# Kernel tuning notes

Hardware: AMD Instinct MI355X
Metric: run time of the kernel (lower is better)

## Reference

```python
import jax, jax.numpy as jnp
import numpy as np

N = 50000
E = 800000
FIN = 128
H = 2
C = 64
OUT = 40
NEG_SLOPE = 0.2
BN_EPS = 1e-5


def setup_inputs() -> dict:
    key = jax.random.key(0)
    ks = jax.random.split(key, 16)
    inv = lambda f: 1.0 / np.sqrt(f)
    return {
        "x": jax.random.normal(ks[0], (N, FIN), jnp.float32),
        "edge_index": jax.random.randint(ks[1], (2, E), 0, N, dtype=jnp.int64),
        "W1": jax.random.normal(ks[2], (FIN, H * C), jnp.float32) * inv(FIN),
        "att_src1": jax.random.normal(ks[3], (H, C), jnp.float32) * inv(C),
        "att_dst1": jax.random.normal(ks[4], (H, C), jnp.float32) * inv(C),
        "b1": jax.random.normal(ks[5], (H * C,), jnp.float32) * 0.1,
        "bn_gamma": jnp.ones((H * C,), jnp.float32),
        "bn_beta": jnp.zeros((H * C,), jnp.float32),
        "bn_mean": jax.random.normal(ks[6], (H * C,), jnp.float32) * 0.1,
        "bn_var": jax.random.uniform(ks[7], (H * C,), jnp.float32) + 0.5,
        "W2": jax.random.normal(ks[8], (H * C, H * C), jnp.float32) * inv(H * C),
        "att_src2": jax.random.normal(ks[9], (H, C), jnp.float32) * inv(C),
        "att_dst2": jax.random.normal(ks[10], (H, C), jnp.float32) * inv(C),
        "b2": jax.random.normal(ks[11], (H * C,), jnp.float32) * 0.1,
        "Wf": jax.random.normal(ks[12], (H * C, OUT), jnp.float32) * inv(H * C),
        "bf": jax.random.normal(ks[13], (OUT,), jnp.float32) * 0.1,
    }


def _gat_conv(x, src, dst, W, att_src, att_dst, b):
    """PyG GATConv (concat=True): per-edge attention, segment softmax over dst, scatter-sum."""
    n = x.shape[0]
    h = (x @ W).reshape(n, H, C)                       # [N,H,C]
    a_src = jnp.sum(h * att_src, axis=-1)              # [N,H]
    a_dst = jnp.sum(h * att_dst, axis=-1)              # [N,H]
    e = jax.nn.leaky_relu(a_src[src] + a_dst[dst], NEG_SLOPE)   # [E,H]
    m = jax.ops.segment_max(e, dst, num_segments=n)    # [N,H]
    m = jnp.where(jnp.isfinite(m), m, 0.0)
    ex = jnp.exp(e - m[dst])                           # [E,H]
    denom = jax.ops.segment_sum(ex, dst, num_segments=n)
    alpha = ex / (denom[dst] + 1e-16)                  # [E,H]
    out = jax.ops.segment_sum(alpha[:, :, None] * h[src], dst, num_segments=n)  # [N,H,C]
    return out.reshape(n, H * C) + b


def reference(x, edge_index, W1, att_src1, att_dst1, b1, bn_gamma, bn_beta,
              bn_mean, bn_var, W2, att_src2, att_dst2, b2, Wf, bf):
    n = x.shape[0]
    # GATConv default add_self_loops=True
    loops = jnp.arange(n, dtype=edge_index.dtype)
    src = jnp.concatenate([edge_index[0], loops])
    dst = jnp.concatenate([edge_index[1], loops])

    x1 = _gat_conv(x, src, dst, W1, att_src1, att_dst1, b1)
    # BatchNorm1d (inference: running stats)
    x1 = (x1 - bn_mean) * jax.lax.rsqrt(bn_var + BN_EPS) * bn_gamma + bn_beta
    x1 = jax.nn.elu(x1)
    # dropout is identity in eval mode
    x2 = _gat_conv(x1, src, dst, W2, att_src2, att_dst2, b2)

    xj = jnp.maximum(x1, x2)                           # JumpingKnowledge 'max'
    logits = xj @ Wf + bf
    return jax.nn.log_softmax(logits, axis=1)
```

## Files before the change

### kernel.cpp

```cpp
#include <hip/hip_runtime.h>

#define NN 50000
#define EE 800000
#define ETOT 850000
#define NEG 0.2f
#define BNEPS 1e-5f
#define OUTC 40
#define MSHIFT 20.0f
#define PSZ 6250
#define NCHUNK 416
#define CHSZ 2044
#define ELLW 64

typedef unsigned short ushort_t;
typedef unsigned char uchar_t;
typedef unsigned int uint32;
typedef long long ll_t;

typedef __attribute__((ext_vector_type(8))) short short8;
typedef __attribute__((ext_vector_type(4))) float f32x4;
typedef __attribute__((ext_vector_type(2))) float f32x2;

__device__ __forceinline__ float bf2f(ushort_t u){ return __uint_as_float(((uint32)u)<<16); }
__device__ __forceinline__ float2 upk2(uint32 v){
  return make_float2(__uint_as_float(v<<16), __uint_as_float(v & 0xffff0000u));
}
__device__ __forceinline__ ushort_t f2bf(float f){
  uint32 u = __float_as_uint(f);
  uint32 r = ((u>>16)&1u) + 0x7fffu;
  return (ushort_t)((u + r)>>16);
}
__device__ __forceinline__ float ldf(const void* p, int i, bool f32){
  return f32 ? ((const float*)p)[i] : bf2f(((const ushort_t*)p)[i]);
}

__device__ __forceinline__ uchar_t enc_fp8(float v){
#if __has_builtin(__builtin_amdgcn_cvt_pk_fp8_f32)
  int p = __builtin_amdgcn_cvt_pk_fp8_f32(v, v, 0, false);
  return (uchar_t)(p & 0xFF);
#else
  float a = fabsf(v);
  uint32 s = (v < 0.f) ? 0x80u : 0u;
  if (a < 0.0009765625f) return (uchar_t)s;
  a = fminf(a, 448.f);
  int e; float m = frexpf(a, &e);
  int E = e + 6;
  uint32 mant;
  if (E <= 0){
    mant = (uint32)lrintf(a * 512.f);
    if (mant > 7) return (uchar_t)(s | 0x08u);
    return (uchar_t)(s | mant);
  }
  mant = (uint32)lrintf(m * 16.f);
  if (mant >= 16){ mant = 8; E += 1; }
  if (E > 15){ E = 15; mant = 14; }
  return (uchar_t)(s | ((uint32)E<<3) | (mant - 8));
#endif
}
__device__ __forceinline__ float2 dec_fp8x2(ushort_t h){
#if __has_builtin(__builtin_amdgcn_cvt_pk_f32_fp8)
  f32x2 r = __builtin_amdgcn_cvt_pk_f32_fp8((uint32)h, false);
  return make_float2(r[0], r[1]);
#else
  float o[2];
  #pragma unroll
  for (int i=0;i<2;i++){
    uint32 v = (h >> (8*i)) & 0xFFu;
    uint32 s = (v & 0x80u) << 24;
    uint32 e = (v >> 3) & 0xFu, m = v & 7u;
    float r = (e == 0) ? ((float)m * 0.001953125f)
                       : __uint_as_float(((e + 120u) << 23) | (m << 20));
    o[i] = __uint_as_float(__float_as_uint(r) | s);
  }
  return make_float2(o[0], o[1]);
#endif
}

__device__ __forceinline__ bool x_is_f32(const void* xp){
  int lane = threadIdx.x & 63;
  uint32 w = ((const uint32*)xp)[lane];
  uint32 e = (w >> 7) & 0xffu;
  unsigned long long b = __ballot(e >= 100u && e <= 140u);
  return __popcll(b) < 48;
}

__device__ __forceinline__ bool ei_is64(const int* __restrict__ ei){
  int lane = threadIdx.x & 63;
  unsigned long long b = __ballot(ei[2*lane + 1] == 0);
  return b == ~0ull;
}
__device__ __forceinline__ int clampn(int v){ return min(max(v, 0), NN-1); }

__global__ __launch_bounds__(256) void econv_k(const int* __restrict__ ei,
                                               int2* __restrict__ ei2, int* __restrict__ cnt){
  bool is64 = ei_is64(ei);
  int b = blockIdx.x;
  if (b >= 3125){
    int idx = (b - 3125)*256 + (int)threadIdx.x;
    if (idx < NN) cnt[idx] = 0;
    return;
  }
  int j = b*256 + (int)threadIdx.x;
  int s, d;
  if (is64){
    s = clampn((int)((const ll_t*)ei)[j]);
    d = clampn((int)((const ll_t*)ei)[EE + j]);
  } else {
    s = clampn(ei[j]); d = clampn(ei[EE + j]);
  }
  ei2[j] = make_int2(s, d);
}

__global__ __launch_bounds__(256) void fill_ell_k(const int2* __restrict__ ei2,
                                                  int* __restrict__ cnt, int* __restrict__ ell){
  int p = blockIdx.x & 7;
  int c = blockIdx.x >> 3;
  int lo = c * CHSZ, hi = min(lo + CHSZ, ETOT);
  for (int j = lo + (int)threadIdx.x; j < hi; j += 256){
    int s, d;
    if (j < EE){ int2 e = ei2[j]; s = e.x; d = e.y; }
    else { s = j - EE; d = s; }
    if (d / PSZ == p){
      int pos = atomicAdd(&cnt[d], 1);
      if (pos < ELLW) ell[d*ELLW + pos] = s;
    }
  }
}

__global__ __launch_bounds__(256) void gemm_k(const void* __restrict__ X, const void* __restrict__ W,
                                              const void* __restrict__ atts, const void* __restrict__ attd,
                                              uchar_t* __restrict__ Hout,
                                              float2* __restrict__ a_src, float2* __restrict__ a_dst,
                                              int nrows, const void* __restrict__ xdet, int xf_en){
  bool f32 = x_is_f32(xdet);
  bool xf = f32 && (xf_en != 0);
  __shared__ ushort_t Bt[128*136];
  int t = threadIdx.x;
  int row0 = blockIdx.x * 128;
  if (f32){
    const float* Wff = (const float*)W;
    #pragma unroll
    for (int i=0;i<64;i++){
      int idx = t + i*256;
      int k = idx >> 7, n = idx & 127;
      Bt[n*136 + k] = f2bf(Wff[idx]);
    }
  } else {
    #pragma unroll
    for (int i=0;i<32;i++){
      int idx = t + i*256;
      int k = idx >> 6;
      int n2 = (idx & 63)*2;
      uint32 val = ((const uint32*)W)[idx];
      Bt[n2*136 + k]     = (ushort_t)(val & 0xffffu);
      Bt[(n2+1)*136 + k] = (ushort_t)(val >> 16);
    }
  }
  __syncthreads();
  int wv = t >> 6, lane = t & 63;
  int quad = lane >> 4, m16 = lane & 15;
  int r0 = row0 + wv*32 + m16;
  int r1 = r0 + 16;
  int rr0 = min(r0, nrows-1), rr1 = min(r1, nrows-1);
  f32x4 acc[2][8];
  #pragma unroll
  for (int a=0;a<2;a++)
    #pragma unroll
    for (int b=0;b<8;b++) acc[a][b] = (f32x4){0.f,0.f,0.f,0.f};
  #pragma unroll
  for (int ks=0; ks<4; ks++){
    int ko = ks*32 + quad*8;
    short8 a0, a1;
    if (xf){
      const float* Xf = (const float*)X;
      float4 q0 = *(const float4*)(Xf + (size_t)rr0*128 + ko);
      float4 q1 = *(const float4*)(Xf + (size_t)rr0*128 + ko + 4);
      float4 p0 = *(const float4*)(Xf + (size_t)rr1*128 + ko);
      float4 p1 = *(const float4*)(Xf + (size_t)rr1*128 + ko + 4);
      a0[0]=(short)f2bf(q0.x); a0[1]=(short)f2bf(q0.y); a0[2]=(short)f2bf(q0.z); a0[3]=(short)f2bf(q0.w);
      a0[4]=(short)f2bf(q1.x); a0[5]=(short)f2bf(q1.y); a0[6]=(short)f2bf(q1.z); a0[7]=(short)f2bf(q1.w);
      a1[0]=(short)f2bf(p0.x); a1[1]=(short)f2bf(p0.y); a1[2]=(short)f2bf(p0.z); a1[3]=(short)f2bf(p0.w);
      a1[4]=(short)f2bf(p1.x); a1[5]=(short)f2bf(p1.y); a1[6]=(short)f2bf(p1.z); a1[7]=(short)f2bf(p1.w);
    } else {
      a0 = *(const short8*)((const ushort_t*)X + (size_t)rr0*128 + ko);
      a1 = *(const short8*)((const ushort_t*)X + (size_t)rr1*128 + ko);
    }
    #pragma unroll
    for (int b=0;b<8;b++){
      short8 bfr = *(const short8*)(&Bt[(b*16 + m16)*136 + ko]);
      acc[0][b] = __builtin_amdgcn_mfma_f32_16x16x32_bf16(a0, bfr, acc[0][b], 0,0,0);
      acc[1][b] = __builtin_amdgcn_mfma_f32_16x16x32_bf16(a1, bfr, acc[1][b], 0,0,0);
    }
  }
  #pragma unroll
  for (int a=0;a<2;a++){
    #pragma unroll
    for (int b=0;b<8;b++){
      #pragma unroll
      for (int i=0;i<4;i++){
        int gr = row0 + wv*32 + a*16 + quad*4 + i;
        int col = b*16 + m16;
        if (gr < nrows) Hout[(size_t)gr*128 + col] = enc_fp8(acc[a][b][i]);
      }
    }
  }
  float aS[8], aD[8];
  #pragma unroll
  for (int b=0;b<8;b++){ aS[b]=ldf(atts, b*16+m16, f32); aD[b]=ldf(attd, b*16+m16, f32); }
  #pragma unroll
  for (int a=0;a<2;a++){
    #pragma unroll
    for (int i=0;i<4;i++){
      float s0v=0.f, s1v=0.f, d0v=0.f, d1v=0.f;
      #pragma unroll
      for (int b=0;b<4;b++){ s0v += acc[a][b][i]*aS[b]; d0v += acc[a][b][i]*aD[b]; }
      #pragma unroll
      for (int b=4;b<8;b++){ s1v += acc[a][b][i]*aS[b]; d1v += acc[a][b][i]*aD[b]; }
      #pragma unroll
      for (int off=1; off<16; off<<=1){
        s0v += __shfl_xor(s0v, off, 64); s1v += __shfl_xor(s1v, off, 64);
        d0v += __shfl_xor(d0v, off, 64); d1v += __shfl_xor(d1v, off, 64);
      }
      int gr = row0 + wv*32 + a*16 + quad*4 + i;
      if (m16 == 0 && gr < nrows){
        a_src[gr] = make_float2(s0v, s1v);
        a_dst[gr] = make_float2(d0v, d1v);
      }
    }
  }
}

template<int LAYER>
__global__ __launch_bounds__(256) void node_k(const int* __restrict__ cnt, const int* __restrict__ ell,
    const float2* __restrict__ a_src, const float2* __restrict__ a_dst, const uchar_t* __restrict__ hmat,
    const void* __restrict__ bias, const void* __restrict__ gamma, const void* __restrict__ beta,
    const void* __restrict__ mean, const void* __restrict__ var,
    ushort_t* __restrict__ xout, const void* __restrict__ xdet){
  bool f32 = x_is_f32(xdet);
  int wv = threadIdx.x >> 6, lane = threadIdx.x & 63;
  int n = blockIdx.x*4 + wv;
  if (n >= NN) return;
  int head = lane >> 5;
  float2 ad = a_dst[n];
  int len = min(cnt[n], ELLW);
  float Dp0 = 0.f, Dp1 = 0.f;
  float accx = 0.f, accy = 0.f;
  const ushort_t* hm = (const ushort_t*)hmat;
  int sv = 0; float w0 = 0.f, w1 = 0.f;
  if (lane < len){
    sv = ell[n*ELLW + lane];
    float2 as = a_src[sv];
    float e0 = as.x + ad.x; e0 = (e0 > 0.f) ? e0 : NEG*e0;
    float e1 = as.y + ad.y; e1 = (e1 > 0.f) ? e1 : NEG*e1;
    w0 = __expf(e0 - MSHIFT);
    w1 = __expf(e1 - MSHIFT);
  }
  Dp0 += w0; Dp1 += w1;
  uint32 wpk = ((uint32)f2bf(w0)) | (((uint32)f2bf(w1)) << 16);
  int e = 0;
  for (; e + 16 <= len; e += 16){
    int sk[16]; uint32 wb[16];
    #pragma unroll
    for (int k=0;k<16;k++){ sk[k] = __shfl(sv, e+k, 64); wb[k] = __shfl(wpk, e+k, 64); }
    ushort_t hv[16];
    #pragma unroll
    for (int k=0;k<16;k++) hv[k] = hm[(size_t)sk[k]*64 + lane];
    #pragma unroll
    for (int k=0;k<16;k++){
      float2 wf = upk2(wb[k]);
      float w = head ? wf.y : wf.x;
      float2 f = dec_fp8x2(hv[k]);
      accx += w*f.x; accy += w*f.y;
    }
  }
  for (; e + 4 <= len; e += 4){
    int sk[4]; uint32 wb[4];
    #pragma unroll
    for (int k=0;k<4;k++){ sk[k] = __shfl(sv, e+k, 64); wb[k] = __shfl(wpk, e+k, 64); }
    ushort_t hv[4];
    #pragma unroll
    for (int k=0;k<4;k++) hv[k] = hm[(size_t)sk[k]*64 + lane];
    #pragma unroll
    for (int k=0;k<4;k++){
      float2 wf = upk2(wb[k]);
      float w = head ? wf.y : wf.x;
      float2 f = dec_fp8x2(hv[k]);
      accx += w*f.x; accy += w*f.y;
    }
  }
  for (; e < len; e++){
    int s = __shfl(sv, e, 64);
    uint32 wbv = __shfl(wpk, e, 64);
    float2 wf = upk2(wbv);
    float w = head ? wf.y : wf.x;
    float2 f = dec_fp8x2(hm[(size_t)s*64 + lane]);
    accx += w*f.x; accy += w*f.y;
  }
  #pragma unroll
  for (int off=1; off<64; off<<=1){
    Dp0 += __shfl_xor(Dp0, off, 64);
    Dp1 += __shfl_xor(Dp1, off, 64);
  }
  float invd = 1.f / ((head ? Dp1 : Dp0) + 1e-16f);
  accx *= invd; accy *= invd;
  int c0i = 2*lane;
  float v0 = accx + ldf(bias, c0i, f32);
  float v1 = accy + ldf(bias, c0i+1, f32);
  if (LAYER == 1){
    v0 = (v0 - ldf(mean,c0i,f32))   * rsqrtf(ldf(var,c0i,f32)   + BNEPS) * ldf(gamma,c0i,f32)   + ldf(beta,c0i,f32);
    v1 = (v1 - ldf(mean,c0i+1,f32)) * rsqrtf(ldf(var,c0i+1,f32) + BNEPS) * ldf(gamma,c0i+1,f32) + ldf(beta,c0i+1,f32);
    v0 = (v0 > 0.f) ? v0 : (__expf(v0) - 1.f);
    v1 = (v1 > 0.f) ? v1 : (__expf(v1) - 1.f);
  }
  uint32 packed = (uint32)f2bf(v0) | ((uint32)f2bf(v1) << 16);
  ((uint32*)xout)[n*64 + lane] = packed;
}

__global__ __launch_bounds__(256) void final_k(const ushort_t* __restrict__ x1, const ushort_t* __restrict__ x2,
    const void* __restrict__ Wf, const void* __restrict__ bfv,
    const void* __restrict__ xdet, void* __restrict__ outp){
  bool f32 = x_is_f32(xdet);
  __shared__ ushort_t Bt[48*136];
  int t = threadIdx.x;
  for (int i = t; i < 48*128; i += 256){
    int n = i >> 7, k = i & 127;
    float v = (n < OUTC) ? ldf(Wf, k*OUTC + n, f32) : 0.f;
    Bt[n*136 + k] = f2bf(v);
  }
  __syncthreads();
  int wv = t >> 6, lane = t & 63;
  int quad = lane >> 4, m16 = lane & 15;
  int row0 = blockIdx.x * 128;
  int r0 = row0 + wv*32 + m16;
  int r1 = r0 + 16;
  int rr0 = min(r0, NN-1), rr1 = min(r1, NN-1);
  f32x4 acc[2][3];
  #pragma unroll
  for (int a=0;a<2;a++)
    #pragma unroll
    for (int b=0;b<3;b++) acc[a][b] = (f32x4){0.f,0.f,0.f,0.f};
  #pragma unroll
  for (int ks=0; ks<4; ks++){
    int ko = ks*32 + quad*8;
    short8 u1 = *(const short8*)(x1 + (size_t)rr0*128 + ko);
    short8 u2 = *(const short8*)(x2 + (size_t)rr0*128 + ko);
    short8 v1 = *(const short8*)(x1 + (size_t)rr1*128 + ko);
    short8 v2 = *(const short8*)(x2 + (size_t)rr1*128 + ko);
    short8 a0, a1;
    #pragma unroll
    for (int j=0;j<8;j++){
      float m0 = fmaxf(bf2f((ushort_t)u1[j]), bf2f((ushort_t)u2[j]));
      float m1 = fmaxf(bf2f((ushort_t)v1[j]), bf2f((ushort_t)v2[j]));
      a0[j] = (short)(__float_as_uint(m0) >> 16);
      a1[j] = (short)(__float_as_uint(m1) >> 16);
    }
    #pragma unroll
    for (int b=0;b<3;b++){
      short8 bfr = *(const short8*)(&Bt[(b*16 + m16)*136 + ko]);
      acc[0][b] = __builtin_amdgcn_mfma_f32_16x16x32_bf16(a0, bfr, acc[0][b], 0,0,0);
      acc[1][b] = __builtin_amdgcn_mfma_f32_16x16x32_bf16(a1, bfr, acc[1][b], 0,0,0);
    }
  }
  float bb[3];
  #pragma unroll
  for (int b=0;b<3;b++){
    int col = b*16 + m16;
    bb[b] = (col < OUTC) ? ldf(bfv, col, f32) : 0.f;
  }
  #pragma unroll
  for (int a=0;a<2;a++){
    #pragma unroll
    for (int i=0;i<4;i++){
      int r = row0 + wv*32 + a*16 + quad*4 + i;
      float L[3];
      #pragma unroll
      for (int b=0;b<3;b++){
        int col = b*16 + m16;
        L[b] = (col < OUTC) ? (acc[a][b][i] + bb[b]) : -1e30f;
      }
      float mx = fmaxf(fmaxf(L[0], L[1]), L[2]);
      #pragma unroll
      for (int off=1; off<16; off<<=1) mx = fmaxf(mx, __shfl_xor(mx, off, 64));
      float s = __expf(L[0]-mx) + __expf(L[1]-mx) + __expf(L[2]-mx);
      #pragma unroll
      for (int off=1; off<16; off<<=1) s += __shfl_xor(s, off, 64);
      float lg = __logf(s);
      if (r < NN){
        #pragma unroll
        for (int b=0;b<3;b++){
          int col = b*16 + m16;
          if (col < OUTC){
            float res = L[b] - mx - lg;
            if (f32) ((float*)outp)[(size_t)r*OUTC + col] = res;
            else     ((ushort_t*)outp)[(size_t)r*OUTC + col] = f2bf(res);
          }
        }
      }
    }
  }
}

extern "C" void kernel_launch(void* const* d_in, const int* in_sizes, int n_in,
                              void* d_out, int out_size, void* d_ws, size_t ws_size,
                              hipStream_t stream){
  const int* ei = (const int*)d_in[1];

  const size_t NEEDED = 52500000ULL;
  if (ws_size < NEEDED) return;

  char* ws = (char*)d_ws;
  size_t off = 0;
  auto alloc = [&](size_t bytes)->void*{
    void* p = ws + off;
    off = (off + bytes + 255) & ~(size_t)255;
    return p;
  };
  int* cnt      = (int*)alloc((size_t)NN*4);
  int* ell      = (int*)alloc((size_t)NN*ELLW*4);
  int2* ei2     = (int2*)alloc((size_t)EE*8);
  float2* a_src = (float2*)alloc((size_t)NN*8);
  float2* a_dst = (float2*)alloc((size_t)NN*8);
  uchar_t* hbuf  = (uchar_t*)alloc((size_t)NN*128);
  ushort_t* x1b  = (ushort_t*)alloc((size_t)NN*128*2);
  ushort_t* x2b  = (ushort_t*)alloc((size_t)NN*128*2);

  econv_k<<<3321, 256, 0, stream>>>(ei, ei2, cnt);
  fill_ell_k<<<NCHUNK*8, 256, 0, stream>>>(ei2, cnt, ell);

  gemm_k<<<(NN+127)/128, 256, 0, stream>>>(d_in[0], d_in[2], d_in[3], d_in[4],
                                           hbuf, a_src, a_dst, NN, d_in[0], 1);
  node_k<1><<<(NN+3)/4, 256, 0, stream>>>(cnt, ell, a_src, a_dst, hbuf,
                                          d_in[5], d_in[6], d_in[7], d_in[8], d_in[9], x1b, d_in[0]);
  gemm_k<<<(NN+127)/128, 256, 0, stream>>>(x1b, d_in[10], d_in[11], d_in[12],
                                           hbuf, a_src, a_dst, NN, d_in[0], 0);
  node_k<2><<<(NN+3)/4, 256, 0, stream>>>(cnt, ell, a_src, a_dst, hbuf,
                                          d_in[13], nullptr, nullptr, nullptr, nullptr, x2b, d_in[0]);

  final_k<<<(NN+127)/128, 256, 0, stream>>>(x1b, x2b, d_in[14], d_in[15], d_in[0], d_out);
}
```

Baseline: 261.1 us.

## Gather fp8 neighbor rows with 16-byte loads, 8 edges per wave

Restructures the per-node aggregation so each wave processes 8 edges at once. Each lane loads a 16-byte chunk of a neighbor's fp8 feature row instead of 2 bytes per lane per edge, and keeps 16 partial accumulators. The partial sums are reduced across sub-groups with shuffles and redistributed through shared memory. The goal is fewer, wider memory transactions and more loads in flight per wave. In exchange it adds register pressure, a 48-shuffle reduction, a shared-memory round trip with __syncthreads, and the n>=NN early return is gone (NN divides evenly by 4, so this is safe).

```diff
diff --git a/kernel.cpp b/kernel.cpp
--- a/kernel.cpp
+++ b/kernel.cpp
@@ -57,17 +57,19 @@
   return (uchar_t)(s | ((uint32)E<<3) | (mant - 8));
 #endif
 }
-__device__ __forceinline__ float2 dec_fp8x2(ushort_t h){
+template<bool HI>
+__device__ __forceinline__ float2 dec_fp8x2w(uint32 v){
 #if __has_builtin(__builtin_amdgcn_cvt_pk_f32_fp8)
-  f32x2 r = __builtin_amdgcn_cvt_pk_f32_fp8((uint32)h, false);
+  f32x2 r = __builtin_amdgcn_cvt_pk_f32_fp8((int)v, HI);
   return make_float2(r[0], r[1]);
 #else
+  uint32 h = HI ? (v >> 16) : (v & 0xFFFFu);
   float o[2];
   #pragma unroll
   for (int i=0;i<2;i++){
-    uint32 v = (h >> (8*i)) & 0xFFu;
-    uint32 s = (v & 0x80u) << 24;
-    uint32 e = (v >> 3) & 0xFu, m = v & 7u;
+    uint32 b = (h >> (8*i)) & 0xFFu;
+    uint32 s = (b & 0x80u) << 24;
+    uint32 e = (b >> 3) & 0xFu, m = b & 7u;
     float r = (e == 0) ? ((float)m * 0.001953125f)
                        : __uint_as_float(((e + 120u) << 23) | (m << 20));
     o[i] = __uint_as_float(__float_as_uint(r) | s);
@@ -237,15 +239,11 @@
     const void* __restrict__ mean, const void* __restrict__ var,
     ushort_t* __restrict__ xout, const void* __restrict__ xdet){
   bool f32 = x_is_f32(xdet);
+  __shared__ float xsh[4][128];
   int wv = threadIdx.x >> 6, lane = threadIdx.x & 63;
   int n = blockIdx.x*4 + wv;
-  if (n >= NN) return;
-  int head = lane >> 5;
   float2 ad = a_dst[n];
   int len = min(cnt[n], ELLW);
-  float Dp0 = 0.f, Dp1 = 0.f;
-  float accx = 0.f, accy = 0.f;
-  const ushort_t* hm = (const ushort_t*)hmat;
   int sv = 0; float w0 = 0.f, w1 = 0.f;
   if (lane < len){
     sv = ell[n*ELLW + lane];
@@ -255,57 +253,66 @@
     w0 = __expf(e0 - MSHIFT);
     w1 = __expf(e1 - MSHIFT);
   }
-  Dp0 += w0; Dp1 += w1;
+  float Dp0 = w0, Dp1 = w1;
   uint32 wpk = ((uint32)f2bf(w0)) | (((uint32)f2bf(w1)) << 16);
-  int e = 0;
-  for (; e + 16 <= len; e += 16){
-    int sk[16]; uint32 wb[16];
-    #pragma unroll
-    for (int k=0;k<16;k++){ sk[k] = __shfl(sv, e+k, 64); wb[k] = __shfl(wpk, e+k, 64); }
-    ushort_t hv[16];
-    #pragma unroll
-    for (int k=0;k<16;k++) hv[k] = hm[(size_t)sk[k]*64 + lane];
-    #pragma unroll
-    for (int k=0;k<16;k++){
-      float2 wf = upk2(wb[k]);
-      float w = head ? wf.y : wf.x;
-      float2 f = dec_fp8x2(hv[k]);
-      accx += w*f.x; accy += w*f.y;
-    }
-  }
-  for (; e + 4 <= len; e += 4){
-    int sk[4]; uint32 wb[4];
-    #pragma unroll
-    for (int k=0;k<4;k++){ sk[k] = __shfl(sv, e+k, 64); wb[k] = __shfl(wpk, e+k, 64); }
-    ushort_t hv[4];
-    #pragma unroll
-    for (int k=0;k<4;k++) hv[k] = hm[(size_t)sk[k]*64 + lane];
+  int sub = lane >> 3;
+  int c   = lane & 7;
+  bool head1 = (c >= 4);
+  float acc[16];
+  #pragma unroll
+  for (int i=0;i<16;i++) acc[i] = 0.f;
+  const uint4* hm4 = (const uint4*)hmat;
+  int ngroups = (len + 7) >> 3;
+  for (int g = 0; g < ngroups; g += 4){
+    int sG[4]; float wG[4];
     #pragma unroll
     for (int k=0;k<4;k++){
-      float2 wf = upk2(wb[k]);
-      float w = head ? wf.y : wf.x;
-      float2 f = dec_fp8x2(hv[k]);
-      accx += w*f.x; accy += w*f.y;
-    }
-  }
-  for (; e < len; e++){
-    int s = __shfl(sv, e, 64);
-    uint32 wbv = __shfl(wpk, e, 64);
-    float2 wf = upk2(wbv);
-    float w = head ? wf.y : wf.x;
-    float2 f = dec_fp8x2(hm[(size_t)s*64 + lane]);
-    accx += w*f.x; accy += w*f.y;
+      int eidx = (g + k)*8 + sub;
+      sG[k] = __shfl(sv, eidx, 64);
+      uint32 wb = __shfl(wpk, eidx, 64);
+      float2 wf = upk2(wb);
+      wG[k] = head1 ? wf.y : wf.x;
+    }
+    uint4 hv[4];
+    #pragma unroll
+    for (int k=0;k<4;k++) hv[k] = hm4[(size_t)sG[k]*8 + c];
+    #pragma unroll
+    for (int k=0;k<4;k++){
+      float w = wG[k];
+      uint32 uu[4] = {hv[k].x, hv[k].y, hv[k].z, hv[k].w};
+      #pragma unroll
+      for (int u=0;u<4;u++){
+        float2 f0 = dec_fp8x2w<false>(uu[u]);
+        float2 f1 = dec_fp8x2w<true>(uu[u]);
+        acc[4*u+0] += w*f0.x; acc[4*u+1] += w*f0.y;
+        acc[4*u+2] += w*f1.x; acc[4*u+3] += w*f1.y;
+      }
+    }
+  }
+  #pragma unroll
+  for (int off=8; off<64; off<<=1){
+    #pragma unroll
+    for (int i=0;i<16;i++) acc[i] += __shfl_xor(acc[i], off, 64);
   }
   #pragma unroll
   for (int off=1; off<64; off<<=1){
     Dp0 += __shfl_xor(Dp0, off, 64);
     Dp1 += __shfl_xor(Dp1, off, 64);
   }
+  if (lane < 8){
+    #pragma unroll
+    for (int i=0;i<16;i+=2)
+      *(float2*)&xsh[wv][lane*16 + i] = make_float2(acc[i], acc[i+1]);
+  }
+  __syncthreads();
+  int head = lane >> 5;
   float invd = 1.f / ((head ? Dp1 : Dp0) + 1e-16f);
-  accx *= invd; accy *= invd;
+  float2 xv = *(float2*)&xsh[wv][2*lane];
+  float v0 = xv.x * invd;
+  float v1 = xv.y * invd;
   int c0i = 2*lane;
-  float v0 = accx + ldf(bias, c0i, f32);
-  float v1 = accy + ldf(bias, c0i+1, f32);
+  v0 += ldf(bias, c0i, f32);
+  v1 += ldf(bias, c0i+1, f32);
   if (LAYER == 1){
     v0 = (v0 - ldf(mean,c0i,f32))   * rsqrtf(ldf(var,c0i,f32)   + BNEPS) * ldf(gamma,c0i,f32)   + ldf(beta,c0i,f32);
     v1 = (v1 - ldf(mean,c0i+1,f32)) * rsqrtf(ldf(var,c0i+1,f32) + BNEPS) * ldf(gamma,c0i+1,f32) + ldf(beta,c0i+1,f32);
```

Result: slower. 275.1 us (+5.3%).

## Bucket edges by destination partition before building the ELL adjacency

Applied to the files above, without the earlier changes.

The edge-conversion kernel now sorts each block's edges into eight destination-partition buckets in shared memory and appends them to per-partition global queues. The ELL fill kernel then reads each queue once, instead of every partition scanning the whole edge list and discarding non-matching edges. Self-loops are written straight into slot 0 of each node's ELL row during initialisation. This removes roughly eightfold redundant edge reads in exchange for shared-memory bucketing, global queue atomics, an extra memset and a fixed queue capacity that could drop edges if a partition overflows.

```diff
diff --git a/kernel.cpp b/kernel.cpp
--- a/kernel.cpp
+++ b/kernel.cpp
@@ -2,15 +2,13 @@
 
 #define NN 50000
 #define EE 800000
-#define ETOT 850000
 #define NEG 0.2f
 #define BNEPS 1e-5f
 #define OUTC 40
 #define MSHIFT 20.0f
 #define PSZ 6250
-#define NCHUNK 416
-#define CHSZ 2044
 #define ELLW 64
+#define QCAP 131072
 
 typedef unsigned short ushort_t;
 typedef unsigned char uchar_t;
@@ -91,16 +89,21 @@
 }
 __device__ __forceinline__ int clampn(int v){ return min(max(v, 0), NN-1); }
 
-__global__ __launch_bounds__(256) void econv_k(const int* __restrict__ ei,
-                                               int2* __restrict__ ei2, int* __restrict__ cnt){
+__global__ __launch_bounds__(256) void econv2_k(const int* __restrict__ ei,
+    int2* __restrict__ q, int* __restrict__ qcnt,
+    int* __restrict__ cnt, int* __restrict__ ell){
   bool is64 = ei_is64(ei);
-  int b = blockIdx.x;
+  int b = blockIdx.x, t = threadIdx.x;
   if (b >= 3125){
-    int idx = (b - 3125)*256 + (int)threadIdx.x;
-    if (idx < NN) cnt[idx] = 0;
+    int idx = (b - 3125)*256 + t;
+    if (idx < NN){ cnt[idx] = 1; ell[idx*ELLW] = idx; }
     return;
   }
-  int j = b*256 + (int)threadIdx.x;
+  __shared__ int2 buck[8][256];
+  __shared__ int bcnt[8], bbase[8];
+  if (t < 8) bcnt[t] = 0;
+  __syncthreads();
+  int j = b*256 + t;
   int s, d;
   if (is64){
     s = clampn((int)((const ll_t*)ei)[j]);
@@ -108,22 +111,32 @@
   } else {
     s = clampn(ei[j]); d = clampn(ei[EE + j]);
   }
-  ei2[j] = make_int2(s, d);
-}
-
-__global__ __launch_bounds__(256) void fill_ell_k(const int2* __restrict__ ei2,
-                                                  int* __restrict__ cnt, int* __restrict__ ell){
+  int p = d / PSZ;
+  int pos = atomicAdd(&bcnt[p], 1);
+  buck[p][pos] = make_int2(s, d);
+  __syncthreads();
+  if (t < 8) bbase[t] = atomicAdd(&qcnt[t], bcnt[t]);
+  __syncthreads();
+  #pragma unroll
+  for (int pp = 0; pp < 8; pp++){
+    int n = bcnt[pp], base = bbase[pp];
+    for (int i = t; i < n; i += 256){
+      int pos2 = base + i;
+      if (pos2 < QCAP) q[(size_t)pp*QCAP + pos2] = buck[pp][i];
+    }
+  }
+}
+
+__global__ __launch_bounds__(256) void fillq_k(const int2* __restrict__ q, const int* __restrict__ qcnt,
+    int* __restrict__ cnt, int* __restrict__ ell){
   int p = blockIdx.x & 7;
-  int c = blockIdx.x >> 3;
-  int lo = c * CHSZ, hi = min(lo + CHSZ, ETOT);
+  int chunk = blockIdx.x >> 3;
+  int qn = min(qcnt[p], QCAP);
+  int lo = chunk*2048, hi = min(lo + 2048, qn);
   for (int j = lo + (int)threadIdx.x; j < hi; j += 256){
-    int s, d;
-    if (j < EE){ int2 e = ei2[j]; s = e.x; d = e.y; }
-    else { s = j - EE; d = s; }
-    if (d / PSZ == p){
-      int pos = atomicAdd(&cnt[d], 1);
-      if (pos < ELLW) ell[d*ELLW + pos] = s;
-    }
+    int2 e = q[(size_t)p*QCAP + j];
+    int pos = atomicAdd(&cnt[e.y], 1);
+    if (pos < ELLW) ell[e.y*ELLW + pos] = e.x;
   }
 }
 
@@ -405,7 +418,7 @@
                               hipStream_t stream){
   const int* ei = (const int*)d_in[1];
 
-  const size_t NEEDED = 52500000ULL;
+  const size_t NEEDED = 54600000ULL;
   if (ws_size < NEEDED) return;
 
   char* ws = (char*)d_ws;
@@ -417,15 +430,18 @@
   };
   int* cnt      = (int*)alloc((size_t)NN*4);
   int* ell      = (int*)alloc((size_t)NN*ELLW*4);
-  int2* ei2     = (int2*)alloc((size_t)EE*8);
+  int2* q       = (int2*)alloc((size_t)8*QCAP*8);
+  int* qcnt     = (int*)alloc(8*4);
   float2* a_src = (float2*)alloc((size_t)NN*8);
   float2* a_dst = (float2*)alloc((size_t)NN*8);
   uchar_t* hbuf  = (uchar_t*)alloc((size_t)NN*128);
   ushort_t* x1b  = (ushort_t*)alloc((size_t)NN*128*2);
   ushort_t* x2b  = (ushort_t*)alloc((size_t)NN*128*2);
 
-  econv_k<<<3321, 256, 0, stream>>>(ei, ei2, cnt);
-  fill_ell_k<<<NCHUNK*8, 256, 0, stream>>>(ei2, cnt, ell);
+  hipMemsetAsync(qcnt, 0, 8*4, stream);
+
+  econv2_k<<<3321, 256, 0, stream>>>(ei, q, qcnt, cnt, ell);
+  fillq_k<<<512, 256, 0, stream>>>(q, qcnt, cnt, ell);
 
   gemm_k<<<(NN+127)/128, 256, 0, stream>>>(d_in[0], d_in[2], d_in[3], d_in[4],
                                            hbuf, a_src, a_dst, NN, d_in[0], 1);
```

After: 298.1 us. 14.1% more time.
